# Kernel optimization log

Hardware: AMD Instinct MI355X
Metric: run time of the kernel (lower is better)

The kernel has to match this reference:

```python
import jax, jax.numpy as jnp
import numpy as np

N, E = 50000, 400000          # nodes, edges
IN, H, OUT = 256, 512, 256    # channels
L, K = 2, 2                   # num_layers, Chebyshev order


def setup_inputs() -> dict:
    key = jax.random.key(0)
    ks = jax.random.split(key, 8)
    x = jax.random.normal(ks[0], (N, IN), jnp.float32)
    edge_index = jax.random.randint(ks[1], (2, E), 0, N)
    in_w = jax.random.normal(ks[2], (IN, H), jnp.float32) / np.float32(np.sqrt(IN))
    in_b = jnp.zeros((H,), jnp.float32)
    # ChebConv has K bias-free Linear layers per conv plus one bias vector
    conv_w = jax.random.normal(ks[3], (L, K, H, H), jnp.float32) / np.float32(np.sqrt(H))
    conv_b = jnp.zeros((L, H), jnp.float32)
    out_w = jax.random.normal(ks[4], (H, OUT), jnp.float32) / np.float32(np.sqrt(H))
    out_b = jnp.zeros((OUT,), jnp.float32)
    return dict(x=x, edge_index=edge_index, in_w=in_w, in_b=in_b,
                conv_w=conv_w, conv_b=conv_b, out_w=out_w, out_b=out_b)


def reference(x, edge_index, in_w, in_b, conv_w, conv_b, out_w, out_b):
    # PyG ChebConv normalization with lambda_max=2 (default):
    #   L_hat = 2/lambda_max * (I - D^{-1/2} A D^{-1/2}) - I = -D^{-1/2} A D^{-1/2}
    # i.e. off-diagonal weights -dinv[row]*w*dinv[col], diagonal 0.
    row, col = edge_index[0], edge_index[1]
    w = jnp.ones((E,), x.dtype)
    deg = jax.ops.segment_sum(w, row, num_segments=N)
    dinv = jnp.where(deg > 0, jax.lax.rsqrt(jnp.maximum(deg, 1e-12)), 0.0).astype(x.dtype)
    norm = -dinv[row] * w * dinv[col]  # [E]

    def prop(h):  # L_hat @ h  (gather from source row, scatter-add to target col)
        return jax.ops.segment_sum(norm[:, None] * h[row], col, num_segments=N)

    # dropout is identity in eval mode; reference is deterministic (eval)
    h = jax.nn.silu(x @ in_w + in_b)
    for l in range(L):
        # Chebyshev recursion, K=2: out = Tx0 @ W0 + (L_hat Tx0) @ W1 + b
        Tx0 = h
        out = Tx0 @ conv_w[l, 0]
        Tx1 = prop(Tx0)
        out = out + Tx1 @ conv_w[l, 1] + conv_b[l]
        h = jax.nn.silu(out)
    return h @ out_w + out_b
```

## Files before the change

### kernel.cpp

```cpp
#include <hip/hip_runtime.h>

#define H512 512

typedef short bf16x8 __attribute__((ext_vector_type(8)));
typedef float f32x4  __attribute__((ext_vector_type(4)));

__device__ __forceinline__ float silu_f(float v) { return v / (1.0f + __expf(-v)); }

__device__ __forceinline__ short f2bf(float f) {
    unsigned u = __float_as_uint(f);
    u = (u + 0x7FFFu + ((u >> 16) & 1u)) >> 16;
    return (short)u;
}
__device__ __forceinline__ float bf2f(short s) {
    return __uint_as_float(((unsigned)(unsigned short)s) << 16);
}

__device__ __forceinline__ int xcd_swz(int b, int nwg) {
    const int NX = 8;
    int q = nwg / NX, rr = nwg % NX;
    int xcd = b % NX, idx = b / NX;
    int base = (xcd < rr) ? xcd * (q + 1) : rr * (q + 1) + (xcd - rr) * q;
    return base + idx;
}


__global__ void hist_kernel(const int* __restrict__ row, const int* __restrict__ col,
                            float* __restrict__ deg, int* __restrict__ cnt, int E) {
    int e = blockIdx.x * blockDim.x + threadIdx.x;
    if (e < E) {
        atomicAdd(&deg[row[e]], 1.0f);
        atomicAdd(&cnt[col[e]], 1);
    }
}

__global__ void dinv_kernel(const float* __restrict__ deg, float* __restrict__ dinv, int n) {
    int i = blockIdx.x * blockDim.x + threadIdx.x;
    if (i < n) {
        float d = deg[i];
        dinv[i] = d > 0.0f ? rsqrtf(fmaxf(d, 1e-12f)) : 0.0f;
    }
}

__global__ __launch_bounds__(256) void bsum_kernel(const int* __restrict__ cnt,
                                                   int* __restrict__ bsum, int n) {
    __shared__ int s[4];
    int i = blockIdx.x * 256 + threadIdx.x;
    int v = (i < n) ? cnt[i] : 0;
    #pragma unroll
    for (int off = 32; off; off >>= 1) v += __shfl_down(v, off, 64);
    if ((threadIdx.x & 63) == 0) s[threadIdx.x >> 6] = v;
    __syncthreads();
    if (threadIdx.x == 0) bsum[blockIdx.x] = s[0] + s[1] + s[2] + s[3];
}

__global__ __launch_bounds__(256) void bscan_kernel(const int* __restrict__ bsum,
                                                    int* __restrict__ boff, int B) {
    __shared__ int s[256];
    int tid = threadIdx.x;
    int v = (tid < B) ? bsum[tid] : 0;
    s[tid] = v;
    __syncthreads();
    #pragma unroll
    for (int off = 1; off < 256; off <<= 1) {
        int t = (tid >= off) ? s[tid - off] : 0;
        __syncthreads();
        s[tid] += t;
        __syncthreads();
    }
    if (tid < B) boff[tid] = s[tid] - v;
}

__global__ __launch_bounds__(256) void cscan_kernel(const int* __restrict__ cnt,
                                                    const int* __restrict__ boff,
                                                    int* __restrict__ ptr,
                                                    int* __restrict__ ptr2, int n, int B) {
    __shared__ int s[256];
    int b = blockIdx.x, tid = threadIdx.x;
    int i = b * 256 + tid;
    int v = (i < n) ? cnt[i] : 0;
    s[tid] = v;
    __syncthreads();
    #pragma unroll
    for (int off = 1; off < 256; off <<= 1) {
        int t = (tid >= off) ? s[tid - off] : 0;
        __syncthreads();
        s[tid] += t;
        __syncthreads();
    }
    int exc = boff[b] + s[tid] - v;
    if (i < n) { ptr[i] = exc; ptr2[i] = exc; }
    if (b == B - 1 && tid == 255) ptr[n] = exc + v;
}

__global__ void scatter_kernel(const int* __restrict__ row, const int* __restrict__ col,
                               const float* __restrict__ dinv, int* __restrict__ ptr2,
                               int* __restrict__ esrc, float* __restrict__ ew, int E) {
    int e = blockIdx.x * blockDim.x + threadIdx.x;
    if (e >= E) return;
    int r = row[e], c = col[e];
    int pos = atomicAdd(&ptr2[c], 1);
    esrc[pos] = r;
    ew[pos]   = -dinv[r] * dinv[c];
}


__global__ void bfshuf_kernel(const float* __restrict__ W, short* __restrict__ Bf,
                              int Ksrc, int Nw, int ktot, int ktoff) {
    int tid = blockIdx.x * blockDim.x + threadIdx.x;
    const int nchunks_src = (Nw / 128) * 2 * (Ksrc / 64) * 8;
    if (tid >= nchunks_src * 64) return;
    int lane = tid & 63;  int rest = tid >> 6;
    int nfrag = rest & 3; rest >>= 2;
    int ks    = rest & 1; rest >>= 1;
    int ktl   = rest % (Ksrc / 64); rest /= (Ksrc / 64);
    int wn    = rest & 1;
    int n128  = rest >> 1;
    int r = lane & 15, g = lane >> 4;
    int colw = n128 * 128 + wn * 64 + nfrag * 16 + r;
    int k0   = ktl * 64 + ks * 32 + g * 8;
    size_t dst = ((size_t)(((n128 * 2 + wn) * ktot + ktoff + ktl) * 8 + ks * 4 + nfrag) * 64 + lane) * 8;
    bf16x8 o;
    #pragma unroll
    for (int j = 0; j < 8; ++j) o[j] = f2bf(W[(size_t)(k0 + j) * Nw + colw]);
    *(bf16x8*)(Bf + dst) = o;
}

__global__ void xconv_kernel(const float* __restrict__ x, short* __restrict__ xb,
                             int Nreal, int Mpad) {
    int tid = blockIdx.x * blockDim.x + threadIdx.x;
    if (tid >= Mpad * 32) return;
    int r = tid >> 5, c8 = (tid & 31) * 8;
    bf16x8 o = {0, 0, 0, 0, 0, 0, 0, 0};
    if (r < Nreal) {
        const float4 f0 = *(const float4*)(x + (size_t)r * 256 + c8);
        const float4 f1 = *(const float4*)(x + (size_t)r * 256 + c8 + 4);
        o[0] = f2bf(f0.x); o[1] = f2bf(f0.y); o[2] = f2bf(f0.z); o[3] = f2bf(f0.w);
        o[4] = f2bf(f1.x); o[5] = f2bf(f1.y); o[6] = f2bf(f1.z); o[7] = f2bf(f1.w);
    }
    *(bf16x8*)(xb + (size_t)r * 256 + c8) = o;
}


__global__ __launch_bounds__(256) void gather_kernel(
    const int* __restrict__ ptr, const int* __restrict__ esrc,
    const float* __restrict__ ew, const short* __restrict__ T,
    short* __restrict__ U, int Nreal, int Mpad)
{
    int t = threadIdx.x;
    int node = blockIdx.x * 4 + (t >> 6);
    if (node >= Mpad) return;
    int q = (t & 63) * 8;
    if (node >= Nreal) {
        bf16x8 z = {0, 0, 0, 0, 0, 0, 0, 0};
        *(bf16x8*)(U + (size_t)node * H512 + q) = z;
        return;
    }
    float acc[8] = {0.f, 0.f, 0.f, 0.f, 0.f, 0.f, 0.f, 0.f};
    const int i1 = ptr[node + 1];
    for (int i = ptr[node]; i < i1; ++i) {
        int s   = esrc[i];
        float w = ew[i];
        bf16x8 tv = *(const bf16x8*)(T + (size_t)s * H512 + q);
        #pragma unroll
        for (int j = 0; j < 8; ++j) acc[j] += w * bf2f(tv[j]);
    }
    bf16x8 o;
    #pragma unroll
    for (int j = 0; j < 8; ++j) o[j] = f2bf(acc[j]);
    *(bf16x8*)(U + (size_t)node * H512 + q) = o;
}


template<int SILU, int F32OUT>
__global__ __launch_bounds__(256, 4) void mfma_gemm(
    const short* __restrict__ A0, const short* __restrict__ A1, int ksplit, int lda,
    const short* __restrict__ Bf,
    void* __restrict__ Cout, int ldc,
    const float* __restrict__ bias, int Mreal, int K, int gx)
{
    __shared__ alignas(16) short As[2][128 * 64];

    const int t    = threadIdx.x;
    const int lane = t & 63;
    const int wid  = t >> 6;

    const int wg = xcd_swz(blockIdx.x, gridDim.x);
    const int m0 = (wg / gx) * 128;
    const int n0 = (wg % gx) * 128;

    const int wm = wid >> 1;
    const int wn = wid & 1;

    const int srow  = lane >> 3;
    const int scol  = (lane & 7) * 16;
    const int corig = scol ^ (srow << 4);
    const int cel   = corig >> 1;

    const int r = lane & 15;
    const int g = lane >> 4;

    const int nt = K >> 6;
    const short* Bw = Bf + (size_t)((n0 >> 7) * 2 + wn) * nt * 4096;

    f32x4 acc[4][4];
    #pragma unroll
    for (int m = 0; m < 4; ++m)
        #pragma unroll
        for (int n = 0; n < 4; ++n)
            acc[m][n] = (f32x4){0.f, 0.f, 0.f, 0.f};

    auto stageA = [&](int buf, int kt) {
        const int k0 = kt * 64;
        const short* Abase = (k0 < ksplit) ? (A0 + k0) : (A1 + (k0 - ksplit));
        #pragma unroll
        for (int i = 0; i < 4; ++i) {
            const int r0 = (wid * 4 + i) * 8;
            const short* ga = Abase + (size_t)(m0 + r0 + srow) * lda + cel;
            __builtin_amdgcn_global_load_lds(
                (const __attribute__((address_space(1))) void*)ga,
                (__attribute__((address_space(3))) void*)(As[buf] + r0 * 64), 16, 0, 0);
        }
    };
    auto loadB = [&](bf16x8* bb, int kt) {
        #pragma unroll
        for (int ks = 0; ks < 2; ++ks)
            #pragma unroll
            for (int n = 0; n < 4; ++n)
                bb[ks * 4 + n] = *(const bf16x8*)(Bw + (size_t)(kt * 8 + ks * 4 + n) * 512 + lane * 8);
    };
    auto mmstep = [&](int cur, const bf16x8* bb) {
        const short* Ab = As[cur];
        #pragma unroll
        for (int ks = 0; ks < 2; ++ks) {
            bf16x8 af[4];
            #pragma unroll
            for (int m = 0; m < 4; ++m) {
                const int rowA = wm * 64 + m * 16 + r;
                const int cb   = (ks * 64 + g * 16) ^ ((rowA & 7) << 4);
                af[m] = *(const bf16x8*)((const char*)Ab + rowA * 128 + cb);
            }
            #pragma unroll
            for (int m = 0; m < 4; ++m)
                #pragma unroll
                for (int n = 0; n < 4; ++n)
                    acc[m][n] = __builtin_amdgcn_mfma_f32_16x16x32_bf16(
                        af[m], bb[ks * 4 + n], acc[m][n], 0, 0, 0);
        }
    };

    bf16x8 b[8];
    stageA(0, 0);
    stageA(1, 1);
    loadB(b, 0);
    __builtin_amdgcn_sched_barrier(0);

    for (int tt = 0; tt < nt; ++tt) {
        asm volatile("s_waitcnt vmcnt(8)" ::: "memory");
        __builtin_amdgcn_s_barrier();
        __builtin_amdgcn_sched_barrier(0);
        mmstep(tt & 1, b);
        __builtin_amdgcn_sched_barrier(0);
        __builtin_amdgcn_s_barrier();
        if (tt + 2 < nt) stageA(tt & 1, tt + 2);
        if (tt + 1 < nt) loadB(b, tt + 1);
        __builtin_amdgcn_sched_barrier(0);
    }

    float bb2[4];
    #pragma unroll
    for (int n = 0; n < 4; ++n) bb2[n] = bias[n0 + wn * 64 + n * 16 + r];

    if (F32OUT) {
        #pragma unroll
        for (int m = 0; m < 4; ++m)
            #pragma unroll
            for (int j = 0; j < 4; ++j) {
                const int rr = m0 + wm * 64 + m * 16 + g * 4 + j;
                #pragma unroll
                for (int n = 0; n < 4; ++n) {
                    float v = acc[m][n][j] + bb2[n];
                    if (SILU) v = silu_f(v);
                    if (rr < Mreal)
                        ((float*)Cout)[(size_t)rr * ldc + n0 + wn * 64 + n * 16 + r] = v;
                }
            }
    } else {
        __syncthreads();
        short* fs = (short*)As;
        #pragma unroll
        for (int m = 0; m < 4; ++m)
            #pragma unroll
            for (int j = 0; j < 4; ++j) {
                const int row = wm * 64 + m * 16 + g * 4 + j;
                const int rot = (row & 15) << 3;
                #pragma unroll
                for (int n = 0; n < 4; ++n) {
                    float v = acc[m][n][j] + bb2[n];
                    if (SILU) v = silu_f(v);
                    const int col = wn * 64 + n * 16 + r;
                    fs[row * 128 + ((col + rot) & 127)] = f2bf(v);
                }
            }
        __syncthreads();
        const int rr   = t >> 1;
        const int hf   = t & 1;
        const int rot2 = (rr & 15) << 3;
        const size_t gr = (size_t)(m0 + rr);
        #pragma unroll
        for (int c8 = 0; c8 < 8; ++c8) {
            const int cbase = hf * 64 + c8 * 8;
            const int cl    = (cbase + rot2) & 127;
            bf16x8 v8 = *(const bf16x8*)&fs[rr * 128 + cl];
            *(bf16x8*)((short*)Cout + gr * ldc + n0 + cbase) = v8;
        }
    }
}


extern "C" void kernel_launch(void* const* d_in, const int* in_sizes, int n_in,
                              void* d_out, int out_size, void* d_ws, size_t ws_size,
                              hipStream_t stream)
{
    const float* x      = (const float*)d_in[0];
    const int*   ei     = (const int*)  d_in[1];
    const float* in_w   = (const float*)d_in[2];
    const float* in_b   = (const float*)d_in[3];
    const float* conv_w = (const float*)d_in[4];
    const float* conv_b = (const float*)d_in[5];
    const float* out_w  = (const float*)d_in[6];
    const float* out_b  = (const float*)d_in[7];

    const int N = in_sizes[0] / 256;
    const int E = in_sizes[1] / 2;
    const int MPAD = ((N + 127) / 128) * 128;
    const int* row = ei;
    const int* col = ei + E;

    char* p = (char*)d_ws;
    short* h0 = (short*)p; p += (size_t)MPAD * H512 * 2;
    short* h1 = (short*)p; p += (size_t)MPAD * H512 * 2;
    short* G  = (short*)p; p += (size_t)MPAD * H512 * 2;
    short* xb = G;
    short* bfi = (short*)p; p += (size_t)512 * 256 * 2;
    short* bfc = (short*)p; p += (size_t)2 * 512 * 1024 * 2;
    short* bfo = (short*)p; p += (size_t)256 * 512 * 2;
    float* deg  = (float*)p; p += (size_t)N * 4;
    float* dinv = (float*)p; p += (size_t)N * 4;
    float* ew   = (float*)p; p += (size_t)E * 4;
    int*   cnt  = (int*)p;   p += (size_t)N * 4;
    int*   ptr  = (int*)p;   p += (size_t)(N + 4) * 4;
    int*   ptr2 = (int*)p;   p += (size_t)N * 4;
    int*   esrc = (int*)p;   p += (size_t)E * 4;
    int*   bsum = (int*)p;   p += (size_t)256 * 4;
    int*   boff = (int*)p;   p += (size_t)256 * 4;

    const int NB = (N + 255) / 256;

    hipMemsetAsync(deg, 0, (size_t)N * sizeof(float), stream);
    hipMemsetAsync(cnt, 0, (size_t)N * sizeof(int), stream);
    hist_kernel<<<(E + 255) / 256, 256, 0, stream>>>(row, col, deg, cnt, E);
    dinv_kernel<<<(N + 255) / 256, 256, 0, stream>>>(deg, dinv, N);
    bsum_kernel <<<NB, 256, 0, stream>>>(cnt, bsum, N);
    bscan_kernel<<<1, 256, 0, stream>>>(bsum, boff, NB);
    cscan_kernel<<<NB, 256, 0, stream>>>(cnt, boff, ptr, ptr2, N, NB);
    scatter_kernel<<<(E + 255) / 256, 256, 0, stream>>>(row, col, dinv, ptr2, esrc, ew, E);

    bfshuf_kernel<<<(512 * 256 / 8 + 255) / 256, 256, 0, stream>>>(in_w, bfi, 256, 512, 4, 0);
    for (int l = 0; l < 2; ++l)
        for (int j = 0; j < 2; ++j)
            bfshuf_kernel<<<(512 * 512 / 8 + 255) / 256, 256, 0, stream>>>(
                conv_w + (size_t)(l * 2 + j) * 512 * 512,
                bfc + (size_t)l * 512 * 1024, 512, 512, 16, j * 8);
    bfshuf_kernel<<<(512 * 256 / 8 + 255) / 256, 256, 0, stream>>>(out_w, bfo, 512, 256, 8, 0);
    xconv_kernel<<<(MPAD * 32 + 255) / 256, 256, 0, stream>>>(x, xb, N, MPAD);

    const int mt = MPAD / 128;

    mfma_gemm<1, 0><<<dim3(4 * mt), 256, 0, stream>>>(
        xb, xb, 256, 256, bfi, h0, H512, in_b, N, 256, 4);

    short* hc = h0;
    short* hn = h1;
    for (int l = 0; l < 2; ++l) {
        gather_kernel<<<(MPAD + 3) / 4, 256, 0, stream>>>(ptr, esrc, ew, hc, G, N, MPAD);
        mfma_gemm<1, 0><<<dim3(4 * mt), 256, 0, stream>>>(
            hc, G, 512, H512, bfc + (size_t)l * 512 * 1024,
            hn, H512, conv_b + (size_t)l * H512, N, 1024, 4);
        short* tmp = hc; hc = hn; hn = tmp;
    }

    mfma_gemm<0, 1><<<dim3(2 * mt), 256, 0, stream>>>(
        hc, hc, 512, H512, bfo, d_out, 256, out_b, N, 512, 2);
}
```

Baseline: 451.7 us.

## Retile GEMM to 256x64 with per-wave private A tiles and no block barriers

The GEMM tile changes from 128x128 (2x2 waves) to 256x64, where each wave owns 64 private rows of A staged into its own LDS region. Because no wave reads another wave's LDS data, the block-wide s_barriers and __syncthreads are dropped and replaced by per-wave waitcnt. The weight shuffle layout is updated to 64-column chunks to match, and M padding moves to 256. The cost is that each wave now loads its own B fragments with no sharing across waves, so B traffic per output doubles, and LDS use per block is higher (launch bounds lowered to 3).

```diff
diff --git a/kernel.cpp b/kernel.cpp
--- a/kernel.cpp
+++ b/kernel.cpp
@@ -108,22 +108,22 @@
 __global__ void bfshuf_kernel(const float* __restrict__ W, short* __restrict__ Bf,
                               int Ksrc, int Nw, int ktot, int ktoff) {
     int tid = blockIdx.x * blockDim.x + threadIdx.x;
-    const int nchunks_src = (Nw / 128) * 2 * (Ksrc / 64) * 8;
-    if (tid >= nchunks_src * 64) return;
+    const int kts = Ksrc / 64;
+    const int nch = (Nw / 64) * kts * 8;
+    if (tid >= nch * 64) return;
     int lane = tid & 63;  int rest = tid >> 6;
-    int nfrag = rest & 3; rest >>= 2;
-    int ks    = rest & 1; rest >>= 1;
-    int ktl   = rest % (Ksrc / 64); rest /= (Ksrc / 64);
-    int wn    = rest & 1;
-    int n128  = rest >> 1;
+    int nf = rest & 3; rest >>= 2;
+    int ks = rest & 1; rest >>= 1;
+    int ktl = rest % kts;
+    int n64 = rest / kts;
     int r = lane & 15, g = lane >> 4;
-    int colw = n128 * 128 + wn * 64 + nfrag * 16 + r;
+    int colw = n64 * 64 + nf * 16 + r;
     int k0   = ktl * 64 + ks * 32 + g * 8;
-    size_t dst = ((size_t)(((n128 * 2 + wn) * ktot + ktoff + ktl) * 8 + ks * 4 + nfrag) * 64 + lane) * 8;
+    size_t chunk = ((size_t)(n64 * ktot + ktoff + ktl) * 2 + ks) * 4 + nf;
     bf16x8 o;
     #pragma unroll
     for (int j = 0; j < 8; ++j) o[j] = f2bf(W[(size_t)(k0 + j) * Nw + colw]);
-    *(bf16x8*)(Bf + dst) = o;
+    *(bf16x8*)(Bf + (chunk * 64 + lane) * 8) = o;
 }
 
 __global__ void xconv_kernel(const float* __restrict__ x, short* __restrict__ xb,
@@ -173,35 +173,31 @@
 
 
 template<int SILU, int F32OUT>
-__global__ __launch_bounds__(256, 4) void mfma_gemm(
+__global__ __launch_bounds__(256, 3) void mfma_gemm(
     const short* __restrict__ A0, const short* __restrict__ A1, int ksplit, int lda,
     const short* __restrict__ Bf,
     void* __restrict__ Cout, int ldc,
     const float* __restrict__ bias, int Mreal, int K, int gx)
 {
-    __shared__ alignas(16) short As[2][128 * 64];
+    __shared__ alignas(16) short lds[2 * 4 * 4096];
 
     const int t    = threadIdx.x;
     const int lane = t & 63;
     const int wid  = t >> 6;
 
     const int wg = xcd_swz(blockIdx.x, gridDim.x);
-    const int m0 = (wg / gx) * 128;
-    const int n0 = (wg % gx) * 128;
-
-    const int wm = wid >> 1;
-    const int wn = wid & 1;
-
-    const int srow  = lane >> 3;
-    const int scol  = (lane & 7) * 16;
-    const int corig = scol ^ (srow << 4);
-    const int cel   = corig >> 1;
+    const int m0 = (wg / gx) * 256;
+    const int n0 = (wg % gx) * 64;
+
+    const int srow = lane >> 3;
+    const int scol = (lane & 7) * 16;
+    const int cel  = (scol ^ (srow << 4)) >> 1;
 
     const int r = lane & 15;
     const int g = lane >> 4;
 
     const int nt = K >> 6;
-    const short* Bw = Bf + (size_t)((n0 >> 7) * 2 + wn) * nt * 4096;
+    const short* Bw = Bf + (size_t)(n0 >> 6) * nt * 4096;
 
     f32x4 acc[4][4];
     #pragma unroll
@@ -213,13 +209,13 @@
     auto stageA = [&](int buf, int kt) {
         const int k0 = kt * 64;
         const short* Abase = (k0 < ksplit) ? (A0 + k0) : (A1 + (k0 - ksplit));
-        #pragma unroll
-        for (int i = 0; i < 4; ++i) {
-            const int r0 = (wid * 4 + i) * 8;
-            const short* ga = Abase + (size_t)(m0 + r0 + srow) * lda + cel;
+        short* dst0 = lds + (buf * 4 + wid) * 4096;
+        #pragma unroll
+        for (int i = 0; i < 8; ++i) {
+            const short* ga = Abase + (size_t)(m0 + wid * 64 + i * 8 + srow) * lda + cel;
             __builtin_amdgcn_global_load_lds(
                 (const __attribute__((address_space(1))) void*)ga,
-                (__attribute__((address_space(3))) void*)(As[buf] + r0 * 64), 16, 0, 0);
+                (__attribute__((address_space(3))) void*)(dst0 + i * 512), 16, 0, 0);
         }
     };
     auto loadB = [&](bf16x8* bb, int kt) {
@@ -227,16 +223,16 @@
         for (int ks = 0; ks < 2; ++ks)
             #pragma unroll
             for (int n = 0; n < 4; ++n)
-                bb[ks * 4 + n] = *(const bf16x8*)(Bw + (size_t)(kt * 8 + ks * 4 + n) * 512 + lane * 8);
+                bb[ks * 4 + n] = *(const bf16x8*)(Bw + (((size_t)(kt * 2 + ks)) * 4 + n) * 512 + lane * 8);
     };
-    auto mmstep = [&](int cur, const bf16x8* bb) {
-        const short* Ab = As[cur];
+    auto mmstep = [&](int buf, const bf16x8* bb) {
+        const short* Ab = lds + (buf * 4 + wid) * 4096;
         #pragma unroll
         for (int ks = 0; ks < 2; ++ks) {
             bf16x8 af[4];
             #pragma unroll
             for (int m = 0; m < 4; ++m) {
-                const int rowA = wm * 64 + m * 16 + r;
+                const int rowA = m * 16 + r;
                 const int cb   = (ks * 64 + g * 16) ^ ((rowA & 7) << 4);
                 af[m] = *(const bf16x8*)((const char*)Ab + rowA * 128 + cb);
             }
@@ -251,68 +247,64 @@
 
     bf16x8 b[8];
     stageA(0, 0);
+    loadB(b, 0);
     stageA(1, 1);
-    loadB(b, 0);
     __builtin_amdgcn_sched_barrier(0);
 
     for (int tt = 0; tt < nt; ++tt) {
-        asm volatile("s_waitcnt vmcnt(8)" ::: "memory");
-        __builtin_amdgcn_s_barrier();
+        if (tt + 1 < nt) asm volatile("s_waitcnt vmcnt(8)" ::: "memory");
+        else             asm volatile("s_waitcnt vmcnt(0)" ::: "memory");
         __builtin_amdgcn_sched_barrier(0);
         mmstep(tt & 1, b);
+        asm volatile("s_waitcnt lgkmcnt(0)" ::: "memory");
         __builtin_amdgcn_sched_barrier(0);
-        __builtin_amdgcn_s_barrier();
+        if (tt + 1 < nt) loadB(b, tt + 1);
         if (tt + 2 < nt) stageA(tt & 1, tt + 2);
-        if (tt + 1 < nt) loadB(b, tt + 1);
         __builtin_amdgcn_sched_barrier(0);
     }
 
     float bb2[4];
     #pragma unroll
-    for (int n = 0; n < 4; ++n) bb2[n] = bias[n0 + wn * 64 + n * 16 + r];
+    for (int n = 0; n < 4; ++n) bb2[n] = bias[n0 + n * 16 + r];
 
     if (F32OUT) {
         #pragma unroll
         for (int m = 0; m < 4; ++m)
             #pragma unroll
             for (int j = 0; j < 4; ++j) {
-                const int rr = m0 + wm * 64 + m * 16 + g * 4 + j;
+                const int rr = m0 + wid * 64 + m * 16 + g * 4 + j;
                 #pragma unroll
                 for (int n = 0; n < 4; ++n) {
                     float v = acc[m][n][j] + bb2[n];
                     if (SILU) v = silu_f(v);
                     if (rr < Mreal)
-                        ((float*)Cout)[(size_t)rr * ldc + n0 + wn * 64 + n * 16 + r] = v;
+                        ((float*)Cout)[(size_t)rr * ldc + n0 + n * 16 + r] = v;
                 }
             }
     } else {
-        __syncthreads();
-        short* fs = (short*)As;
+        short* fs = lds + wid * 4096;
         #pragma unroll
         for (int m = 0; m < 4; ++m)
             #pragma unroll
             for (int j = 0; j < 4; ++j) {
-                const int row = wm * 64 + m * 16 + g * 4 + j;
-                const int rot = (row & 15) << 3;
+                const int row = m * 16 + g * 4 + j;
+                const int rot = (row & 7) << 3;
                 #pragma unroll
                 for (int n = 0; n < 4; ++n) {
                     float v = acc[m][n][j] + bb2[n];
                     if (SILU) v = silu_f(v);
-                    const int col = wn * 64 + n * 16 + r;
-                    fs[row * 128 + ((col + rot) & 127)] = f2bf(v);
+                    fs[row * 64 + ((n * 16 + r + rot) & 63)] = f2bf(v);
                 }
             }
-        __syncthreads();
-        const int rr   = t >> 1;
-        const int hf   = t & 1;
-        const int rot2 = (rr & 15) << 3;
-        const size_t gr = (size_t)(m0 + rr);
+        asm volatile("s_waitcnt lgkmcnt(0)" ::: "memory");
+        __builtin_amdgcn_sched_barrier(0);
+        const int rot2 = (lane & 7) << 3;
+        const size_t gr = (size_t)(m0 + wid * 64 + lane);
         #pragma unroll
         for (int c8 = 0; c8 < 8; ++c8) {
-            const int cbase = hf * 64 + c8 * 8;
-            const int cl    = (cbase + rot2) & 127;
-            bf16x8 v8 = *(const bf16x8*)&fs[rr * 128 + cl];
-            *(bf16x8*)((short*)Cout + gr * ldc + n0 + cbase) = v8;
+            const int cl = (c8 * 8 + rot2) & 63;
+            bf16x8 v8 = *(const bf16x8*)&fs[lane * 64 + cl];
+            *(bf16x8*)((short*)Cout + gr * ldc + n0 + c8 * 8) = v8;
         }
     }
 }
@@ -333,7 +325,7 @@
 
     const int N = in_sizes[0] / 256;
     const int E = in_sizes[1] / 2;
-    const int MPAD = ((N + 127) / 128) * 128;
+    const int MPAD = ((N + 255) / 256) * 256;
     const int* row = ei;
     const int* col = ei + E;
 
@@ -366,30 +358,30 @@
     cscan_kernel<<<NB, 256, 0, stream>>>(cnt, boff, ptr, ptr2, N, NB);
     scatter_kernel<<<(E + 255) / 256, 256, 0, stream>>>(row, col, dinv, ptr2, esrc, ew, E);
 
-    bfshuf_kernel<<<(512 * 256 / 8 + 255) / 256, 256, 0, stream>>>(in_w, bfi, 256, 512, 4, 0);
+    bfshuf_kernel<<<(8 * 4 * 8 * 64 + 255) / 256, 256, 0, stream>>>(in_w, bfi, 256, 512, 4, 0);
     for (int l = 0; l < 2; ++l)
         for (int j = 0; j < 2; ++j)
-            bfshuf_kernel<<<(512 * 512 / 8 + 255) / 256, 256, 0, stream>>>(
+            bfshuf_kernel<<<(8 * 8 * 8 * 64 + 255) / 256, 256, 0, stream>>>(
                 conv_w + (size_t)(l * 2 + j) * 512 * 512,
                 bfc + (size_t)l * 512 * 1024, 512, 512, 16, j * 8);
-    bfshuf_kernel<<<(512 * 256 / 8 + 255) / 256, 256, 0, stream>>>(out_w, bfo, 512, 256, 8, 0);
+    bfshuf_kernel<<<(4 * 8 * 8 * 64 + 255) / 256, 256, 0, stream>>>(out_w, bfo, 512, 256, 8, 0);
     xconv_kernel<<<(MPAD * 32 + 255) / 256, 256, 0, stream>>>(x, xb, N, MPAD);
 
-    const int mt = MPAD / 128;
-
-    mfma_gemm<1, 0><<<dim3(4 * mt), 256, 0, stream>>>(
-        xb, xb, 256, 256, bfi, h0, H512, in_b, N, 256, 4);
+    const int mt = MPAD / 256;
+
+    mfma_gemm<1, 0><<<dim3(8 * mt), 256, 0, stream>>>(
+        xb, xb, 256, 256, bfi, h0, H512, in_b, N, 256, 8);
 
     short* hc = h0;
     short* hn = h1;
     for (int l = 0; l < 2; ++l) {
         gather_kernel<<<(MPAD + 3) / 4, 256, 0, stream>>>(ptr, esrc, ew, hc, G, N, MPAD);
-        mfma_gemm<1, 0><<<dim3(4 * mt), 256, 0, stream>>>(
+        mfma_gemm<1, 0><<<dim3(8 * mt), 256, 0, stream>>>(
             hc, G, 512, H512, bfc + (size_t)l * 512 * 1024,
-            hn, H512, conv_b + (size_t)l * H512, N, 1024, 4);
+            hn, H512, conv_b + (size_t)l * H512, N, 1024, 8);
         short* tmp = hc; hc = hn; hn = tmp;
     }
 
-    mfma_gemm<0, 1><<<dim3(2 * mt), 256, 0, stream>>>(
-        hc, hc, 512, H512, bfo, d_out, 256, out_b, N, 512, 2);
-}
+    mfma_gemm<0, 1><<<dim3(4 * mt), 256, 0, stream>>>(
+        hc, hc, 512, H512, bfo, d_out, 256, out_b, N, 512, 4);
+}
```

New measurement: 492.4 us. +9.0%, slower.
